# Optimization experiments

Hardware: AMD Instinct MI355X
Metric: run time of the kernel (lower is better)

The kernel has to match this reference:

```python
import jax, jax.numpy as jnp
from jax import lax
import numpy as np

PARAM_SPECS = [
    ("w1", (16, 15, 5, 5)), ("b1", (16,)),
    ("w2", (32, 16, 3, 3)), ("b2", (32,)),
    ("w3", (32, 32, 3, 3)), ("b3", (32,)),
    ("w4", (32, 32, 3, 3)), ("b4", (32,)),
    ("w5", (64, 32, 3, 3)), ("b5", (64,)),
    ("w6", (32, 96, 3, 3)), ("b6", (32,)),
    ("w7", (32, 64, 3, 3)), ("b7", (32,)),
    ("w8", (32, 64, 3, 3)), ("b8", (32,)),
    ("w9", (64, 48, 3, 3)), ("b9", (64,)),
    ("wi", (16, 15, 3, 3)), ("bi", (16,)),
    ("wo", (3, 16, 3, 3)), ("bo", (3,)),
]


def conv2d(x, w, b, pad):
    y = lax.conv_general_dilated(x, w, (1, 1), [(pad, pad), (pad, pad)],
                                 dimension_numbers=("NCHW", "OIHW", "NCHW"))
    return y + b[None, :, None, None]


def maxpool2(x):
    return lax.reduce_window(x, -jnp.inf, lax.max, (1, 1, 2, 2), (1, 1, 2, 2), "VALID")


def upsample(x, hw):
    # bilinear, half-pixel centers == torch align_corners=False
    B, C = x.shape[:2]
    return jax.image.resize(x, (B, C, hw[0], hw[1]), method="bilinear")


def dcnn(img, p):
    x1 = jax.nn.relu(conv2d(img, p["w1"], p["b1"], 2))
    x2 = jax.nn.relu(conv2d(maxpool2(x1), p["w2"], p["b2"], 1))
    x3 = jax.nn.relu(conv2d(maxpool2(x2), p["w3"], p["b3"], 1))
    x4 = jax.nn.relu(conv2d(maxpool2(x3), p["w4"], p["b4"], 1))
    x5 = jax.nn.relu(conv2d(maxpool2(x4), p["w5"], p["b5"], 1))
    x6 = jax.nn.relu(conv2d(jnp.concatenate([upsample(x5, x4.shape[-2:]), x4], 1), p["w6"], p["b6"], 1))
    x7 = jax.nn.relu(conv2d(jnp.concatenate([upsample(x6, x3.shape[-2:]), x3], 1), p["w7"], p["b7"], 1))
    x8 = jax.nn.relu(conv2d(jnp.concatenate([upsample(x7, x2.shape[-2:]), x2], 1), p["w8"], p["b8"], 1))
    x9 = conv2d(jnp.concatenate([upsample(x8, x1.shape[-2:]), x1], 1), p["w9"], p["b9"], 1)
    return x9


def lrnn_op(X, P, axis, flip):
    # h_k = (1-P_k)*X_k + P_k*h_{k-1}, scanned along `axis`.
    # For reverse directions the torch code stacks hidden states in scan
    # order (spatially flipped) -> flip inputs, scan forward, keep order.
    if flip:
        X = jnp.flip(X, axis)
        P = jnp.flip(P, axis)
    xs = jnp.moveaxis(X, axis, 0)  # [L, B, 16, n]
    ps = jnp.moveaxis(P, axis, 0)

    def step(h, xp):
        x, p = xp
        h = (1.0 - p) * x + p * h
        return h, h

    h0 = jnp.zeros_like(xs[0])
    _, ys = lax.scan(step, h0, (xs, ps))
    return jnp.moveaxis(ys, 0, axis)


def lrnn_layer(x_in, fm):
    dirs = [(0, 3, False), (0, 3, True), (16, 2, False), (16, 2, True),
            (32, 3, False), (32, 3, True), (48, 2, False), (48, 2, True)]
    outs = [lrnn_op(x_in, fm[:, c:c + 16], axis, flip) for (c, axis, flip) in dirs]
    return jnp.max(jnp.stack(outs, axis=1), axis=1)


def setup_inputs() -> dict:
    key = jax.random.key(0)
    ks = jax.random.split(key, len(PARAM_SPECS) + 1)
    inp = {"img": jax.random.normal(ks[0], (8, 15, 256, 256), jnp.float32)}
    for i, (name, shape) in enumerate(PARAM_SPECS):
        inp[name] = jax.random.normal(ks[i + 1], shape, jnp.float32) * 0.05
    return inp


def reference(img, w1, b1, w2, b2, w3, b3, w4, b4, w5, b5, w6, b6, w7, b7,
              w8, b8, w9, b9, wi, bi, wo, bo):
    p = dict(w1=w1, b1=b1, w2=w2, b2=b2, w3=w3, b3=b3, w4=w4, b4=b4, w5=w5,
             b5=b5, w6=w6, b6=b6, w7=w7, b7=b7, w8=w8, b8=b8, w9=w9, b9=b9)
    fm = jnp.tanh(dcnn(img, p))          # [B,64,H,W]
    x_in = conv2d(img, wi, bi, 1)         # [B,16,H,W]
    out = lrnn_layer(x_in, fm)            # [B,16,H,W]
    return jax.nn.sigmoid(conv2d(out, wo, bo, 1))  # [B,3,H,W]
```

## Files before the change

### kernel.cpp

```cpp
#include <hip/hip_runtime.h>
#include <math.h>

typedef __attribute__((ext_vector_type(8)))  short bf16x8;
typedef __attribute__((ext_vector_type(8)))  unsigned short u16x8;
typedef __attribute__((ext_vector_type(16))) float f32x16;

__device__ __forceinline__ unsigned short f2bf(float f) {
    unsigned u = __float_as_uint(f);
    unsigned r = (u + 0x7FFFu + ((u >> 16) & 1u)) >> 16;
    return (unsigned short)r;
}
__device__ __forceinline__ float bf2f(unsigned short h) {
    return __uint_as_float(((unsigned)h) << 16);
}
__device__ __forceinline__ unsigned pack2(unsigned short a, unsigned short b) {
    return (unsigned)a | ((unsigned)b << 16);
}
__device__ __forceinline__ float fast_tanh(float x) {
    float e = __expf(2.f * x);
    return 1.f - 2.f / (e + 1.f);
}

__device__ __forceinline__ void bilin_setup(int y, int x, int Hi, int Wi,
                                            int& i00, int& i01, int& i10, int& i11,
                                            float& wy, float& wx)
{
    float fy = 0.5f * y - 0.25f;
    float fx = 0.5f * x - 0.25f;
    float y0f = floorf(fy), x0f = floorf(fx);
    wy = fy - y0f; wx = fx - x0f;
    int yA = (int)y0f, xA = (int)x0f;
    int yB = yA + 1, xB = xA + 1;
    yA = yA < 0 ? 0 : (yA > Hi - 1 ? Hi - 1 : yA);
    yB = yB < 0 ? 0 : (yB > Hi - 1 ? Hi - 1 : yB);
    xA = xA < 0 ? 0 : (xA > Wi - 1 ? Wi - 1 : xA);
    xB = xB < 0 ? 0 : (xB > Wi - 1 ? Wi - 1 : xB);
    i00 = yA * Wi + xA; i01 = yA * Wi + xB;
    i10 = yB * Wi + xA; i11 = yB * Wi + xB;
}

__device__ __forceinline__ void up2_setup(int v, int Hi, int& i0, int& i1, float& w)
{
    int a = (v - 1) >> 1;
    i0 = a < 0 ? 0 : a;
    int b = a + 1;
    i1 = b > Hi - 1 ? Hi - 1 : b;
    w = (v & 1) ? 0.25f : 0.75f;
}

__device__ __forceinline__ u16x8 bilin8(const unsigned short* __restrict__ sb,
                                        int i00, int i01, int i10, int i11,
                                        float wy, float wx, int stride)
{
    u16x8 v00 = *(const u16x8*)(sb + (size_t)i00 * stride);
    u16x8 v01 = *(const u16x8*)(sb + (size_t)i01 * stride);
    u16x8 v10 = *(const u16x8*)(sb + (size_t)i10 * stride);
    u16x8 v11 = *(const u16x8*)(sb + (size_t)i11 * stride);
    float w00 = (1.f - wy) * (1.f - wx), w01 = (1.f - wy) * wx;
    float w10 = wy * (1.f - wx),         w11 = wy * wx;
    u16x8 r;
#pragma unroll
    for (int j = 0; j < 8; ++j)
        r[j] = f2bf(w00 * bf2f(v00[j]) + w01 * bf2f(v01[j]) +
                    w10 * bf2f(v10[j]) + w11 * bf2f(v11[j]));
    return r;
}

__device__ const float ALPH[3][2][3][3] = {
    { { {0.f,0.f,0.f},      {0.f,1.f,0.f},       {0.f,0.75f,0.25f} },
      { {0.f,1.f,0.f},      {0.f,0.75f,0.25f},   {0.f,0.25f,0.75f} } },
    { { {0.75f,0.25f,0.f},  {0.25f,0.75f,0.f},   {0.f,0.75f,0.25f} },
      { {0.25f,0.75f,0.f},  {0.f,0.75f,0.25f},   {0.f,0.25f,0.75f} } },
    { { {0.75f,0.25f,0.f},  {0.25f,0.75f,0.f},   {0.f,1.f,0.f} },
      { {0.25f,0.75f,0.f},  {0.f,1.f,0.f},       {0.f,0.f,0.f} } }
};

__global__ void imgT_bf16(const float* __restrict__ img, unsigned short* __restrict__ dst)
{
    int idx = blockIdx.x * 256 + threadIdx.x;
    if (idx >= 8 * 256 * 256) return;
    int x = idx & 255, y = (idx >> 8) & 255, b = idx >> 16;
    unsigned short v[16];
#pragma unroll
    for (int c = 0; c < 15; ++c)
        v[c] = f2bf(img[(size_t)(b * 15 + c) * 65536 + y * 256 + x]);
    v[15] = 0;
    uint4 lo = make_uint4(pack2(v[0], v[1]), pack2(v[2], v[3]), pack2(v[4], v[5]), pack2(v[6], v[7]));
    uint4 hi = make_uint4(pack2(v[8], v[9]), pack2(v[10], v[11]), pack2(v[12], v[13]), pack2(v[14], v[15]));
    *(uint4*)(dst + (size_t)idx * 16)     = lo;
    *(uint4*)(dst + (size_t)idx * 16 + 8) = hi;
}

__device__ __forceinline__ void pack33(const float* __restrict__ w,
                                       unsigned short* __restrict__ dst,
                                       int i, int Cin, int Cout)
{
    int KST = Cin >> 4, MT = Cout >> 5;
    int j = i & 7;
    int lane = (i >> 3) & 63;
    int t = i >> 9;
    int mt = t % MT; t /= MT;
    int kst = t % KST;
    int s = t / KST;
    int oc = mt * 32 + (lane & 31);
    int ci = kst * 16 + (lane >> 5) * 8 + j;
    dst[i] = f2bf(w[(oc * Cin + ci) * 9 + s]);
}

__global__ void wprep_mega(const float* __restrict__ w9, const float* __restrict__ w8,
                           const float* __restrict__ w1, const float* __restrict__ wi,
                           const float* __restrict__ wo, const float* __restrict__ w2,
                           const float* __restrict__ w3, const float* __restrict__ w4,
                           const float* __restrict__ w5, const float* __restrict__ w6,
                           const float* __restrict__ w7,
                           unsigned short* __restrict__ wpk9, unsigned short* __restrict__ wpk8,
                           unsigned short* __restrict__ wpk1, unsigned short* __restrict__ wpki,
                           unsigned short* __restrict__ wpko, unsigned short* __restrict__ wpk2,
                           unsigned short* __restrict__ wpk3, unsigned short* __restrict__ wpk4,
                           unsigned short* __restrict__ wpk5, unsigned short* __restrict__ wpk6,
                           unsigned short* __restrict__ wpk7, unsigned short* __restrict__ wpk9e)
{
    int idx = blockIdx.x * 256 + threadIdx.x;
    if (idx < 27648)       pack33(w9, wpk9, idx, 48, 64);
    else if (idx < 46080)  pack33(w8, wpk8, idx - 27648, 64, 32);
    else if (idx < 58880) {
        int i = idx - 46080;
        int j = i & 7;
        int lane = (i >> 3) & 63;
        int s = i >> 9;
        int oc = lane & 31;
        int ci = (lane >> 5) * 8 + j;
        float v = 0.f;
        if (oc < 16 && ci < 15) v = w1[((oc * 15 + ci) * 5 + s / 5) * 5 + s % 5];
        wpk1[i] = f2bf(v);
    } else if (idx < 63488) {
        int i = idx - 58880;
        int j = i & 7;
        int lane = (i >> 3) & 63;
        int s = i >> 9;
        int oc = lane & 31;
        int ci = (lane >> 5) * 8 + j;
        float v = 0.f;
        if (oc < 16 && ci < 15) v = wi[((oc * 15 + ci) * 3 + s / 3) * 3 + s % 3];
        wpki[i] = f2bf(v);
    } else if (idx < 68096) {
        int i = idx - 63488;
        int j = i & 7;
        int lane = (i >> 3) & 63;
        int s = i >> 9;
        int oc = lane & 31;
        int ci = (lane >> 5) * 8 + j;
        float v = 0.f;
        if (oc < 3) v = wo[((oc * 16 + ci) * 3 + s / 3) * 3 + s % 3];
        wpko[i] = f2bf(v);
    }
    else if (idx < 72704)  pack33(w2, wpk2, idx - 68096, 16, 32);
    else if (idx < 81920)  pack33(w3, wpk3, idx - 72704, 32, 32);
    else if (idx < 91136)  pack33(w4, wpk4, idx - 81920, 32, 32);
    else if (idx < 109568) pack33(w5, wpk5, idx - 91136, 32, 64);
    else if (idx < 137216) pack33(w6, wpk6, idx - 109568, 96, 32);
    else if (idx < 155648) pack33(w7, wpk7, idx - 137216, 64, 32);
    else if (idx < 266240) {
        int i = idx - 155648;
        int j = i & 7;
        int lane = (i >> 3) & 63;
        int t = i >> 9;
        int half = t & 1; t >>= 1;
        int kst  = t & 1; t >>= 1;
        int s    = t % 9; t /= 9;
        int py   = t & 1;
        int cls  = t >> 1;
        int dr = s / 3, dx = s % 3;
        int oc = half * 32 + (lane & 31);
        int ci = kst * 16 + (lane >> 5) * 8 + j;
        float v = 0.f;
#pragma unroll
        for (int dy = 0; dy < 3; ++dy)
            v += ALPH[cls][py][dy][dr] * w9[((oc * 48 + ci) * 3 + dy) * 3 + dx];
        wpk9e[i] = f2bf(v);
    }
}

template<int CIN, int COUT, int H, int W, int ROWS, int POOL>
__global__ __launch_bounds__(256)
void convN_mfma(const unsigned short* __restrict__ in,
                const unsigned short* __restrict__ wpk,
                const float* __restrict__ bias,
                unsigned short* __restrict__ out)
{
    constexpr int G = CIN / 8;
    constexpr int KST = CIN / 16;
    constexpr int MT = COUT / 32;
    constexpr int TR = ROWS + 2;
    constexpr int TWd = W + 2;
    constexpr int PS = TR * TWd * 8 + 8;
    __shared__ __align__(16) unsigned short smem[G * PS];

    const int tid  = threadIdx.x;
    const int lane = tid & 63;
    const int wv   = tid >> 6;
    const int q    = lane >> 5;
    const int y0   = blockIdx.x * ROWS;
    const int b    = blockIdx.y;

    for (int i = tid; i < G * TR * TWd; i += 256) {
        int g = i % G;
        int u = (i / G) % TWd;
        int t = i / (G * TWd);
        int yg = y0 + t - 1, xg = u - 1;
        u16x8 v = {0, 0, 0, 0, 0, 0, 0, 0};
        if (yg >= 0 && yg < H && xg >= 0 && xg < W) {
            if (POOL) {
                const unsigned short* q0 =
                    in + (((size_t)(b * 2 * H + 2 * yg) * 2 * W + 2 * xg) * CIN + g * 8);
                u16x8 a0 = *(const u16x8*)q0;
                u16x8 a1 = *(const u16x8*)(q0 + CIN);
                u16x8 a2 = *(const u16x8*)(q0 + (size_t)2 * W * CIN);
                u16x8 a3 = *(const u16x8*)(q0 + (size_t)2 * W * CIN + CIN);
#pragma unroll
                for (int j = 0; j < 8; ++j)
                    v[j] = f2bf(fmaxf(fmaxf(bf2f(a0[j]), bf2f(a1[j])),
                                      fmaxf(bf2f(a2[j]), bf2f(a3[j]))));
            } else {
                v = *(const u16x8*)(in + (((size_t)(b * H + yg) * W + xg) * CIN + g * 8));
            }
        }
        *(u16x8*)(&smem[g * PS + (t * TWd + u) * 8]) = v;
    }
    __syncthreads();

    const int p = wv * 32 + (lane & 31);
    const int r = p / W;
    const int x = p % W;

    f32x16 acc[MT];
#pragma unroll
    for (int mt = 0; mt < MT; ++mt)
#pragma unroll
        for (int i = 0; i < 16; ++i) acc[mt][i] = 0.f;

    const unsigned short* wbase = wpk + lane * 8;

#pragma unroll
    for (int s = 0; s < 9; ++s) {
        const int dy = s / 3, dx = s % 3;
#pragma unroll
        for (int kst = 0; kst < KST; ++kst) {
            const int g = kst * 2 + q;
            bf16x8 bfrag = *(const bf16x8*)(&smem[g * PS + ((r + dy) * TWd + (x + dx)) * 8]);
#pragma unroll
            for (int mt = 0; mt < MT; ++mt) {
                bf16x8 a = *(const bf16x8*)(wbase + ((s * KST + kst) * MT + mt) * 512);
                acc[mt] = __builtin_amdgcn_mfma_f32_32x32x16_bf16(a, bfrag, acc[mt], 0, 0, 0);
            }
        }
    }

    size_t base = ((size_t)(b * H + y0 + r) * W + x) * COUT;
#pragma unroll
    for (int mt = 0; mt < MT; ++mt)
#pragma unroll
        for (int rg = 0; rg < 4; ++rg) {
            int oc = mt * 32 + 8 * rg + 4 * q;
            unsigned short s0 = f2bf(fmaxf(acc[mt][rg * 4 + 0] + bias[oc + 0], 0.f));
            unsigned short s1 = f2bf(fmaxf(acc[mt][rg * 4 + 1] + bias[oc + 1], 0.f));
            unsigned short s2 = f2bf(fmaxf(acc[mt][rg * 4 + 2] + bias[oc + 2], 0.f));
            unsigned short s3 = f2bf(fmaxf(acc[mt][rg * 4 + 3] + bias[oc + 3], 0.f));
            *(uint2*)(out + base + oc) = make_uint2(pack2(s0, s1), pack2(s2, s3));
        }
}

template<int UPC, int CSKIP, int COUT, int H, int W, int ROWS>
__global__ __launch_bounds__(256)
void convU_mfma(const unsigned short* __restrict__ up,
                const unsigned short* __restrict__ skip,
                const unsigned short* __restrict__ wpk,
                const float* __restrict__ bias,
                unsigned short* __restrict__ out)
{
    constexpr int CIN = UPC + CSKIP;
    constexpr int G = CIN / 8;
    constexpr int GU = UPC / 8;
    constexpr int KST = CIN / 16;
    constexpr int MT = COUT / 32;
    constexpr int TR = ROWS + 2;
    constexpr int TWd = W + 2;
    constexpr int PS = TR * TWd * 8 + 8;
    __shared__ __align__(16) unsigned short smem[G * PS];

    const int tid  = threadIdx.x;
    const int lane = tid & 63;
    const int wv   = tid >> 6;
    const int q    = lane >> 5;
    const int y0   = blockIdx.x * ROWS;
    const int b    = blockIdx.y;

    for (int i = tid; i < G * TR * TWd; i += 256) {
        int g = i % G;
        int u = (i / G) % TWd;
        int t = i / (G * TWd);
        int yg = y0 + t - 1, xg = u - 1;
        u16x8 v = {0, 0, 0, 0, 0, 0, 0, 0};
        if (yg >= 0 && yg < H && xg >= 0 && xg < W) {
            if (g < GU) {
                int i00, i01, i10, i11; float wy, wx;
                bilin_setup(yg, xg, H / 2, W / 2, i00, i01, i10, i11, wy, wx);
                v = bilin8(up + (size_t)b * (H / 2) * (W / 2) * UPC + g * 8,
                           i00, i01, i10, i11, wy, wx, UPC);
            } else {
                v = *(const u16x8*)(skip + (((size_t)(b * H + yg) * W + xg) * CSKIP
                                            + (g - GU) * 8));
            }
        }
        *(u16x8*)(&smem[g * PS + (t * TWd + u) * 8]) = v;
    }
    __syncthreads();

    const int p = wv * 32 + (lane & 31);
    const int r = p / W;
    const int x = p % W;

    f32x16 acc[MT];
#pragma unroll
    for (int mt = 0; mt < MT; ++mt)
#pragma unroll
        for (int i = 0; i < 16; ++i) acc[mt][i] = 0.f;

    const unsigned short* wbase = wpk + lane * 8;

#pragma unroll
    for (int s = 0; s < 9; ++s) {
        const int dy = s / 3, dx = s % 3;
#pragma unroll
        for (int kst = 0; kst < KST; ++kst) {
            const int g = kst * 2 + q;
            bf16x8 bfrag = *(const bf16x8*)(&smem[g * PS + ((r + dy) * TWd + (x + dx)) * 8]);
#pragma unroll
            for (int mt = 0; mt < MT; ++mt) {
                bf16x8 a = *(const bf16x8*)(wbase + ((s * KST + kst) * MT + mt) * 512);
                acc[mt] = __builtin_amdgcn_mfma_f32_32x32x16_bf16(a, bfrag, acc[mt], 0, 0, 0);
            }
        }
    }

    size_t base = ((size_t)(b * H + y0 + r) * W + x) * COUT;
#pragma unroll
    for (int mt = 0; mt < MT; ++mt)
#pragma unroll
        for (int rg = 0; rg < 4; ++rg) {
            int oc = mt * 32 + 8 * rg + 4 * q;
            unsigned short s0 = f2bf(fmaxf(acc[mt][rg * 4 + 0] + bias[oc + 0], 0.f));
            unsigned short s1 = f2bf(fmaxf(acc[mt][rg * 4 + 1] + bias[oc + 1], 0.f));
            unsigned short s2 = f2bf(fmaxf(acc[mt][rg * 4 + 2] + bias[oc + 2], 0.f));
            unsigned short s3 = f2bf(fmaxf(acc[mt][rg * 4 + 3] + bias[oc + 3], 0.f));
            *(uint2*)(out + base + oc) = make_uint2(pack2(s0, s1), pack2(s2, s3));
        }
}

__global__ __launch_bounds__(256)
void conv1i_mfma(const unsigned short* __restrict__ imgT,
                 const unsigned short* __restrict__ wpk1,
                 const unsigned short* __restrict__ wpki,
                 const float* __restrict__ b1, const float* __restrict__ bi,
                 unsigned short* __restrict__ x1t, unsigned short* __restrict__ xin)
{
    __shared__ __align__(16) unsigned short smem[2 * 5 * 132 * 8];

    const int tid  = threadIdx.x;
    const int lane = tid & 63;
    const int wv   = tid >> 6;
    const int n    = lane & 31;
    const int q    = lane >> 5;
    const int y    = blockIdx.x >> 1;
    const int x0   = (blockIdx.x & 1) * 128;
    const int b    = blockIdx.y;

    for (int i = tid; i < 5 * 132 * 2; i += 256) {
        int r   = i / 264;
        int rem = i - r * 264;
        int xi  = rem >> 1;
        int g   = rem & 1;
        int yg = y + r - 2;
        int xg = x0 - 2 + xi;
        uint4 v = make_uint4(0, 0, 0, 0);
        if (yg >= 0 && yg < 256 && xg >= 0 && xg < 256)
            v = *(const uint4*)(imgT + (((size_t)(b * 256 + yg) * 256 + xg) * 16 + g * 8));
        *(uint4*)(&smem[((g * 5 + r) * 132 + xi) * 8]) = v;
    }
    __syncthreads();

    f32x16 acc1, acci;
#pragma unroll
    for (int i = 0; i < 16; ++i) { acc1[i] = 0.f; acci[i] = 0.f; }

    const int pxl = wv * 32 + n;
    const unsigned short* wb1 = wpk1 + lane * 8;
    const unsigned short* wbi = wpki + lane * 8;

#pragma unroll
    for (int s = 0; s < 25; ++s) {
        const int dy = s / 5, dx = s % 5;
        bf16x8 bfrag = *(const bf16x8*)(&smem[((q * 5 + dy) * 132 + pxl + dx) * 8]);
        bf16x8 a = *(const bf16x8*)(wb1 + s * 512);
        acc1 = __builtin_amdgcn_mfma_f32_32x32x16_bf16(a, bfrag, acc1, 0, 0, 0);
    }
#pragma unroll
    for (int s = 0; s < 9; ++s) {
        const int dy = s / 3, dx = s % 3;
        bf16x8 bfrag = *(const bf16x8*)(&smem[((q * 5 + dy + 1) * 132 + pxl + dx + 1) * 8]);
        bf16x8 a = *(const bf16x8*)(wbi + s * 512);
        acci = __builtin_amdgcn_mfma_f32_32x32x16_bf16(a, bfrag, acci, 0, 0, 0);
    }

    const int px = x0 + pxl;
    size_t base1 = ((size_t)(b * 256 + y) * 256 + px) * 16;
#pragma unroll
    for (int rg = 0; rg < 2; ++rg) {
        int oc = 8 * rg + 4 * q;
        unsigned short s0 = f2bf(fmaxf(acc1[rg * 4 + 0] + b1[oc + 0], 0.f));
        unsigned short s1 = f2bf(fmaxf(acc1[rg * 4 + 1] + b1[oc + 1], 0.f));
        unsigned short s2 = f2bf(fmaxf(acc1[rg * 4 + 2] + b1[oc + 2], 0.f));
        unsigned short s3 = f2bf(fmaxf(acc1[rg * 4 + 3] + b1[oc + 3], 0.f));
        *(uint2*)(x1t + base1 + oc) = make_uint2(pack2(s0, s1), pack2(s2, s3));
    }
#pragma unroll
    for (int reg = 0; reg < 8; ++reg) {
        int row = (reg & 3) + 8 * (reg >> 2) + 4 * q;
        xin[((size_t)(b * 16 + row) * 256 + y) * 256 + px] = f2bf(acci[reg] + bi[row]);
    }
}

__global__ __launch_bounds__(256)
void conv8_mfma(const unsigned short* __restrict__ x7t,
                const unsigned short* __restrict__ x2t,
                const unsigned short* __restrict__ wpk8,
                const float* __restrict__ bias,
                unsigned short* __restrict__ x8t)
{
    constexpr int PS8 = 4 * 66 * 8 + 8;
    __shared__ __align__(16) unsigned short smem[8 * PS8];

    const int tid  = threadIdx.x;
    const int lane = tid & 63;
    const int wv   = tid >> 6;
    const int n    = lane & 31;
    const int q    = lane >> 5;
    const int x0   = (blockIdx.x & 1) * 64;
    const int yp   = blockIdx.x >> 1;
    const int b    = blockIdx.y;

    for (int i = tid; i < 8 * 4 * 66; i += 256) {
        int t   = i / 528;
        int rem = i - t * 528;
        int xi  = rem >> 3;
        int g   = rem & 7;
        int yg = 2 * yp + t - 1;
        int xg = x0 - 1 + xi;
        u16x8 v = {0, 0, 0, 0, 0, 0, 0, 0};
        if (yg >= 0 && yg < 128 && xg >= 0 && xg < 128) {
            if (g < 4) {
                int iy0, iy1, ix0, ix1; float wy, wx;
                up2_setup(yg, 64, iy0, iy1, wy);
                up2_setup(xg, 64, ix0, ix1, wx);
                v = bilin8(x7t + (size_t)b * 64 * 64 * 32 + g * 8,
                           iy0 * 64 + ix0, iy0 * 64 + ix1,
                           iy1 * 64 + ix0, iy1 * 64 + ix1, wy, wx, 32);
            } else {
                v = *(const u16x8*)(x2t + (((size_t)(b * 128 + yg) * 128 + xg) * 32
                                           + (g - 4) * 8));
            }
        }
        *(u16x8*)(&smem[g * PS8 + (t * 66 + xi) * 8]) = v;
    }
    __syncthreads();

    const int rr  = wv >> 1;
    const int pxl = (wv & 1) * 32 + n;

    f32x16 acc;
#pragma unroll
    for (int i = 0; i < 16; ++i) acc[i] = 0.f;

    const unsigned short* wbase = wpk8 + lane * 8;

#pragma unroll
    for (int s = 0; s < 9; ++s) {
        const int dy = s / 3, dx = s % 3;
#pragma unroll
        for (int kst = 0; kst < 4; ++kst) {
            const int g = kst * 2 + q;
            bf16x8 bfrag = *(const bf16x8*)(&smem[g * PS8 + ((rr + dy) * 66 + pxl + dx) * 8]);
            bf16x8 a = *(const bf16x8*)(wbase + (s * 4 + kst) * 512);
            acc = __builtin_amdgcn_mfma_f32_32x32x16_bf16(a, bfrag, acc, 0, 0, 0);
        }
    }

    size_t base = ((size_t)(b * 128 + 2 * yp + rr) * 128 + x0 + pxl) * 32;
#pragma unroll
    for (int rg = 0; rg < 4; ++rg) {
        int oc0 = 8 * rg + 4 * q;
        unsigned short s0 = f2bf(fmaxf(acc[rg * 4 + 0] + bias[oc0 + 0], 0.f));
        unsigned short s1 = f2bf(fmaxf(acc[rg * 4 + 1] + bias[oc0 + 1], 0.f));
        unsigned short s2 = f2bf(fmaxf(acc[rg * 4 + 2] + bias[oc0 + 2], 0.f));
        unsigned short s3 = f2bf(fmaxf(acc[rg * 4 + 3] + bias[oc0 + 3], 0.f));
        *(uint2*)(x8t + base + oc0) = make_uint2(pack2(s0, s1), pack2(s2, s3));
    }
}

__global__ __launch_bounds__(256)
void conv9f_mfma(const unsigned short* __restrict__ x8t,
                 const unsigned short* __restrict__ x1t,
                 const unsigned short* __restrict__ wpk,
                 const unsigned short* __restrict__ wpk9e,
                 const float* __restrict__ bias,
                 unsigned short* __restrict__ fm)
{
    constexpr int PS8X = 3 * 66 * 8 + 8;
    constexpr int PS1  = 4 * 66 * 8 + 8;
    constexpr int X1OFF = 4 * PS8X;
    __shared__ __align__(16) unsigned short smem[4 * PS8X + 2 * PS1];

    const int tid  = threadIdx.x;
    const int lane = tid & 63;
    const int wv   = tid >> 6;
    const int n    = lane & 31;
    const int q    = lane >> 5;
    const int x0   = (blockIdx.x & 3) * 64;
    const int yp   = blockIdx.x >> 2;
    const int b    = blockIdx.y;

    for (int i = tid; i < 792 + 528; i += 256) {
        if (i < 792) {
            int g   = i & 3;
            int rem = i >> 2;
            int xi  = rem % 66;
            int t8  = rem / 66;
            int r   = yp - 1 + t8;
            int xg  = x0 - 1 + xi;
            u16x8 v = {0, 0, 0, 0, 0, 0, 0, 0};
            if (r >= 0 && r < 128 && xg >= 0 && xg < 256) {
                int ix0, ix1; float wx;
                up2_setup(xg, 128, ix0, ix1, wx);
                const unsigned short* S = x8t + ((size_t)(b * 128 + r) * 128) * 32 + g * 8;
                u16x8 a0 = *(const u16x8*)(S + ix0 * 32);
                u16x8 a1 = *(const u16x8*)(S + ix1 * 32);
                float w1x = 1.f - wx;
#pragma unroll
                for (int j = 0; j < 8; ++j)
                    v[j] = f2bf(w1x * bf2f(a0[j]) + wx * bf2f(a1[j]));
            }
            *(u16x8*)(&smem[g * PS8X + (t8 * 66 + xi) * 8]) = v;
        } else {
            int jI  = i - 792;
            int g   = jI & 1;
            int rem = jI >> 1;
            int xi  = rem % 66;
            int t   = rem / 66;
            int yg  = 2 * yp + t - 1;
            int xg  = x0 - 1 + xi;
            uint4 v = make_uint4(0, 0, 0, 0);
            if (yg >= 0 && yg < 256 && xg >= 0 && xg < 256)
                v = *(const uint4*)(x1t + (((size_t)(b * 256 + yg) * 256 + xg) * 16 + g * 8));
            *(uint4*)(&smem[X1OFF + g * PS1 + (t * 66 + xi) * 8]) = v;
        }
    }
    __syncthreads();

    const int rr  = wv >> 1;
    const int pxl = (wv & 1) * 32 + n;

    f32x16 acc0, acc1;
#pragma unroll
    for (int i = 0; i < 16; ++i) { acc0[i] = 0.f; acc1[i] = 0.f; }

    const int cls = (yp == 0) ? 0 : ((yp == 127) ? 2 : 1);
    const unsigned short* wE  = wpk9e + (size_t)(cls * 2 + rr) * 18432 + lane * 8;
    const unsigned short* w2b = wpk + lane * 8;

#pragma unroll
    for (int s = 0; s < 9; ++s) {
        const int dr = s / 3, dxx = s % 3;
#pragma unroll
        for (int kst = 0; kst < 2; ++kst) {
            const int g = kst * 2 + q;
            bf16x8 bfrag = *(const bf16x8*)(&smem[g * PS8X + (dr * 66 + pxl + dxx) * 8]);
            bf16x8 a0 = *(const bf16x8*)(wE + ((s * 2 + kst) * 2 + 0) * 512);
            bf16x8 a1 = *(const bf16x8*)(wE + ((s * 2 + kst) * 2 + 1) * 512);
            acc0 = __builtin_amdgcn_mfma_f32_32x32x16_bf16(a0, bfrag, acc0, 0, 0, 0);
            acc1 = __builtin_amdgcn_mfma_f32_32x32x16_bf16(a1, bfrag, acc1, 0, 0, 0);
        }
        {
            bf16x8 bfrag = *(const bf16x8*)(&smem[X1OFF + q * PS1 + ((rr + dr) * 66 + pxl + dxx) * 8]);
            bf16x8 a0 = *(const bf16x8*)(w2b + ((s * 3 + 2) * 2 + 0) * 512);
            bf16x8 a1 = *(const bf16x8*)(w2b + ((s * 3 + 2) * 2 + 1) * 512);
            acc0 = __builtin_amdgcn_mfma_f32_32x32x16_bf16(a0, bfrag, acc0, 0, 0, 0);
            acc1 = __builtin_amdgcn_mfma_f32_32x32x16_bf16(a1, bfrag, acc1, 0, 0, 0);
        }
    }

    __syncthreads();
    unsigned short* lout = smem;
    const int pb = rr * 64 + pxl + q * 512;
#pragma unroll
    for (int reg = 0; reg < 16; ++reg) {
        const int rbase = (reg & 3) + 8 * (reg >> 2);
        lout[rbase * 128 + pb]        = f2bf(fast_tanh(acc0[reg] + bias[rbase + 4 * q]));
        lout[(rbase + 32) * 128 + pb] = f2bf(fast_tanh(acc1[reg] + bias[rbase + 4 * q + 32]));
    }
    __syncthreads();

    const size_t fmb = (size_t)b * 64 * 65536 + (size_t)(2 * yp) * 256 + x0;
    for (int i = tid; i < 1024; i += 256) {
        int oc  = i >> 4;
        int p0  = (i & 15) * 8;
        int rr2 = p0 >> 6;
        int pl  = p0 & 63;
        uint4 v = *(const uint4*)(lout + oc * 128 + p0);
        *(uint4*)(fm + fmb + (size_t)oc * 65536 + rr2 * 256 + pl) = v;
    }
}

__device__ __forceinline__ int X2C(int x) { return x + (x >> 5); }

__global__ __launch_bounds__(256)
void lrnn_w_seg(const unsigned short* __restrict__ X, const unsigned short* __restrict__ FM,
                unsigned short* __restrict__ rnnW)
{
    __shared__ float tx[3][16][264];
    __shared__ unsigned short outm[2][16][256];
    __shared__ float segres[2][16][8][4];
    __shared__ float hin[2][16][8][2];

    const int tid = threadIdx.x;
    const int bid = blockIdx.x;
    const int yt = bid & 15;
    const int c  = (bid >> 4) & 15;
    const int b  = bid >> 8;
    const int y0 = yt * 16;

    const size_t xb  = ((size_t)(b * 16 + c) * 256 + y0) * 256;
    const size_t p1b = ((size_t)(b * 64 + c) * 256 + y0) * 256;
    const size_t p2b = ((size_t)(b * 64 + 32 + c) * 256 + y0) * 256;

    for (int i = tid; i < 1536; i += 256) {
        int s = i >> 9;
        int r = i & 511;
        int y = r >> 5;
        int g = r & 31;
        const unsigned short* sp = (s == 0) ? (X + xb) : (s == 1 ? FM + p1b : FM + p2b);
        u16x8 v = *(const u16x8*)(sp + (size_t)y * 256 + g * 8);
        int c0 = X2C(g * 8);
#pragma unroll
        for (int j = 0; j < 8; ++j) tx[s][y][c0 + j] = bf2f(v[j]);
    }
    __syncthreads();

    const int y  = tid & 15;
    const int sg = (tid >> 4) & 7;
    const int d  = tid >> 7;

    {
        float h1 = 0.f, h2 = 0.f, A1 = 1.f, A2 = 1.f;
        if (d == 0) {
            int cs = X2C(sg * 32);
#pragma unroll
            for (int i = 0; i < 32; ++i) {
                float xv = tx[0][y][cs + i], p1 = tx[1][y][cs + i], p2 = tx[2][y][cs + i];
                h1 = fmaf(p1, h1 - xv, xv); A1 *= p1;
                h2 = fmaf(p2, h2 - xv, xv); A2 *= p2;
            }
        } else {
            int cs = X2C(255 - sg * 32);
#pragma unroll
            for (int i = 0; i < 32; ++i) {
                float xv = tx[0][y][cs - i], p1 = tx[1][y][cs - i], p2 = tx[2][y][cs - i];
                h1 = fmaf(p1, h1 - xv, xv); A1 *= p1;
                h2 = fmaf(p2, h2 - xv, xv); A2 *= p2;
            }
        }
        segres[d][y][sg][0] = h1; segres[d][y][sg][1] = A1;
        segres[d][y][sg][2] = h2; segres[d][y][sg][3] = A2;
    }
    __syncthreads();

    if (tid < 32) {
        int yy = tid & 15, dd = tid >> 4;
        float c1 = 0.f, c2 = 0.f;
        for (int s = 0; s < 8; ++s) {
            hin[dd][yy][s][0] = c1;
            hin[dd][yy][s][1] = c2;
            c1 = segres[dd][yy][s][0] + segres[dd][yy][s][1] * c1;
            c2 = segres[dd][yy][s][2] + segres[dd][yy][s][3] * c2;
        }
    }
    __syncthreads();

    {
        float h1 = hin[d][y][sg][0], h2 = hin[d][y][sg][1];
        if (d == 0) {
            int cs = X2C(sg * 32);
            int xs = sg * 32;
#pragma unroll
            for (int i = 0; i < 32; ++i) {
                float xv = tx[0][y][cs + i], p1 = tx[1][y][cs + i], p2 = tx[2][y][cs + i];
                h1 = fmaf(p1, h1 - xv, xv);
                h2 = fmaf(p2, h2 - xv, xv);
                outm[0][y][xs + i] = f2bf(fmaxf(h1, h2));
            }
        } else {
            int cs = X2C(255 - sg * 32);
#pragma unroll
            for (int i = 0; i < 32; ++i) {
                int t = sg * 32 + i;
                float xv = tx[0][y][cs - i], p1 = tx[1][y][cs - i], p2 = tx[2][y][cs - i];
                h1 = fmaf(p1, h1 - xv, xv);
                h2 = fmaf(p2, h2 - xv, xv);
                outm[1][y][t] = f2bf(fmaxf(h1, h2));
            }
        }
    }
    __syncthreads();

    for (int i = tid; i < 4096; i += 256) {
        int x = i & 255, yy = i >> 8;
        float m = fmaxf(bf2f(outm[0][yy][x]), bf2f(outm[1][yy][x]));
        rnnW[xb + (size_t)yy * 256 + x] = f2bf(m);
    }
}

__global__ __launch_bounds__(256)
void lrnn_h_seg(const unsigned short* __restrict__ X, const unsigned short* __restrict__ FM,
                unsigned short* __restrict__ rnnH)
{
    __shared__ float tx[3][264][17];
    __shared__ unsigned short outm[2][256][16];
    __shared__ float segres[2][16][8][4];
    __shared__ float hin[2][16][8][2];

    const int tid = threadIdx.x;
    const int bid = blockIdx.x;
    const int xt = bid & 15;
    const int c  = (bid >> 4) & 15;
    const int b  = bid >> 8;
    const int x0 = xt * 16;

    const size_t xb  = (size_t)(b * 16 + c) * 65536 + x0;
    const size_t p1b = (size_t)(b * 64 + 16 + c) * 65536 + x0;
    const size_t p2b = (size_t)(b * 64 + 48 + c) * 65536 + x0;

    for (int i = tid; i < 1536; i += 256) {
        int s = i >> 9;
        int r = i & 511;
        int y = r >> 1;
        int g = r & 1;
        const unsigned short* sp = (s == 0) ? (X + xb) : (s == 1 ? FM + p1b : FM + p2b);
        u16x8 v = *(const u16x8*)(sp + (size_t)y * 256 + g * 8);
        int pr = y + (y >> 5);
#pragma unroll
        for (int j = 0; j < 8; ++j) tx[s][pr][g * 8 + j] = bf2f(v[j]);
    }
    __syncthreads();

    const int x  = tid & 15;
    const int sg = (tid >> 4) & 7;
    const int d  = tid >> 7;

    {
        float h1 = 0.f, h2 = 0.f, A1 = 1.f, A2 = 1.f;
        if (d == 0) {
            int rs = X2C(sg * 32);
#pragma unroll
            for (int i = 0; i < 32; ++i) {
                float xv = tx[0][rs + i][x], p1 = tx[1][rs + i][x], p2 = tx[2][rs + i][x];
                h1 = fmaf(p1, h1 - xv, xv); A1 *= p1;
                h2 = fmaf(p2, h2 - xv, xv); A2 *= p2;
            }
        } else {
            int rs = X2C(255 - sg * 32);
#pragma unroll
            for (int i = 0; i < 32; ++i) {
                float xv = tx[0][rs - i][x], p1 = tx[1][rs - i][x], p2 = tx[2][rs - i][x];
                h1 = fmaf(p1, h1 - xv, xv); A1 *= p1;
                h2 = fmaf(p2, h2 - xv, xv); A2 *= p2;
            }
        }
        segres[d][x][sg][0] = h1; segres[d][x][sg][1] = A1;
        segres[d][x][sg][2] = h2; segres[d][x][sg][3] = A2;
    }
    __syncthreads();

    if (tid < 32) {
        int xx = tid & 15, dd = tid >> 4;
        float c1 = 0.f, c2 = 0.f;
        for (int s = 0; s < 8; ++s) {
            hin[dd][xx][s][0] = c1;
            hin[dd][xx][s][1] = c2;
            c1 = segres[dd][xx][s][0] + segres[dd][xx][s][1] * c1;
            c2 = segres[dd][xx][s][2] + segres[dd][xx][s][3] * c2;
        }
    }
    __syncthreads();

    {
        float h1 = hin[d][x][sg][0], h2 = hin[d][x][sg][1];
        if (d == 0) {
            int rs = X2C(sg * 32);
            int ys = sg * 32;
#pragma unroll
            for (int i = 0; i < 32; ++i) {
                float xv = tx[0][rs + i][x], p1 = tx[1][rs + i][x], p2 = tx[2][rs + i][x];
                h1 = fmaf(p1, h1 - xv, xv);
                h2 = fmaf(p2, h2 - xv, xv);
                outm[0][ys + i][x] = f2bf(fmaxf(h1, h2));
            }
        } else {
            int rs = X2C(255 - sg * 32);
#pragma unroll
            for (int i = 0; i < 32; ++i) {
                int t = sg * 32 + i;
                float xv = tx[0][rs - i][x], p1 = tx[1][rs - i][x], p2 = tx[2][rs - i][x];
                h1 = fmaf(p1, h1 - xv, xv);
                h2 = fmaf(p2, h2 - xv, xv);
                outm[1][t][x] = f2bf(fmaxf(h1, h2));
            }
        }
    }
    __syncthreads();

    for (int i = tid; i < 4096; i += 256) {
        int xx = i & 15, yy = i >> 4;
        float m = fmaxf(bf2f(outm[0][yy][xx]), bf2f(outm[1][yy][xx]));
        rnnH[xb + (size_t)yy * 256 + xx] = f2bf(m);
    }
}

__global__ __launch_bounds__(256)
void convo_mfma(const unsigned short* __restrict__ rnnW,
                const unsigned short* __restrict__ rnnH,
                const unsigned short* __restrict__ wpko,
                const float* __restrict__ bo,
                float* __restrict__ outp)
{
    __shared__ __align__(16) unsigned short smem[2 * 3 * 130 * 8];

    const int tid  = threadIdx.x;
    const int lane = tid & 63;
    const int wv   = tid >> 6;
    const int n    = lane & 31;
    const int q    = lane >> 5;
    const int y    = blockIdx.x >> 1;
    const int x0   = (blockIdx.x & 1) * 128;
    const int b    = blockIdx.y;

    for (int i = tid; i < 3 * 16 * 130; i += 256) {
        int xi = i % 130;
        int t  = i / 130;
        int ch = t & 15;
        int r  = t >> 4;
        int yg = y + r - 1;
        int xg = x0 - 1 + xi;
        unsigned short m = 0;
        if (yg >= 0 && yg < 256 && xg >= 0 && xg < 256) {
            size_t off = (size_t)(b * 16 + ch) * 65536 + yg * 256 + xg;
            m = f2bf(fmaxf(bf2f(rnnW[off]), bf2f(rnnH[off])));
        }
        int g = ch >> 3, j = ch & 7;
        smem[((g * 3 + r) * 130 + xi) * 8 + j] = m;
    }
    __syncthreads();

    f32x16 acc;
#pragma unroll
    for (int i = 0; i < 16; ++i) acc[i] = 0.f;

    const int pxl = wv * 32 + n;
    const unsigned short* wbase = wpko + lane * 8;

#pragma unroll
    for (int s = 0; s < 9; ++s) {
        const int dy = s / 3, dx = s % 3;
        bf16x8 bfrag = *(const bf16x8*)(&smem[((q * 3 + dy) * 130 + pxl + dx) * 8]);
        bf16x8 a = *(const bf16x8*)(wbase + s * 512);
        acc = __builtin_amdgcn_mfma_f32_32x32x16_bf16(a, bfrag, acc, 0, 0, 0);
    }

    const int px = x0 + pxl;
    if (q == 0) {
#pragma unroll
        for (int oc = 0; oc < 3; ++oc) {
            float r = acc[oc] + bo[oc];
            outp[((size_t)(b * 3 + oc) * 256 + y) * 256 + px] = 1.f / (1.f + __expf(-r));
        }
    }
}

extern "C" void kernel_launch(void* const* d_in, const int* in_sizes, int n_in,
                              void* d_out, int out_size, void* d_ws, size_t ws_size,
                              hipStream_t stream)
{
    const float* img = (const float*)d_in[0];
    const float* w1 = (const float*)d_in[1];  const float* b1 = (const float*)d_in[2];
    const float* w2 = (const float*)d_in[3];  const float* b2 = (const float*)d_in[4];
    const float* w3 = (const float*)d_in[5];  const float* b3 = (const float*)d_in[6];
    const float* w4 = (const float*)d_in[7];  const float* b4 = (const float*)d_in[8];
    const float* w5 = (const float*)d_in[9];  const float* b5 = (const float*)d_in[10];
    const float* w6 = (const float*)d_in[11]; const float* b6 = (const float*)d_in[12];
    const float* w7 = (const float*)d_in[13]; const float* b7 = (const float*)d_in[14];
    const float* w8 = (const float*)d_in[15]; const float* b8 = (const float*)d_in[16];
    const float* w9 = (const float*)d_in[17]; const float* b9 = (const float*)d_in[18];
    const float* wi = (const float*)d_in[19]; const float* bi = (const float*)d_in[20];
    const float* wo = (const float*)d_in[21]; const float* bo = (const float*)d_in[22];

    char* wsb = (char*)d_ws;
    const size_t MB = (size_t)(1u << 20);
    unsigned short* imgT  = (unsigned short*)(wsb);
    unsigned short* x1t   = (unsigned short*)(wsb + 16 * MB);
    unsigned short* x2t   = (unsigned short*)(wsb + 32 * MB);
    unsigned short* x3t   = (unsigned short*)(wsb + 40 * MB);
    unsigned short* x4t   = (unsigned short*)(wsb + 42 * MB);
    unsigned short* x5t   = (unsigned short*)(wsb + 43 * MB);
    unsigned short* x6t   = (unsigned short*)(wsb + 46 * MB);
    unsigned short* x7t   = (unsigned short*)(wsb + 51 * MB);
    unsigned short* x8t   = (unsigned short*)(wsb + 70 * MB);
    unsigned short* fm16  = (unsigned short*)(wsb + 112 * MB);
    unsigned short* xin16 = (unsigned short*)(wsb + 176 * MB);
    unsigned short* rnnW  = (unsigned short*)(wsb);
    unsigned short* rnnH  = (unsigned short*)(wsb + 16 * MB);
    unsigned short* wpk9 = (unsigned short*)(wsb + 192 * MB);
    unsigned short* wpk8 = wpk9 + 27648;
    unsigned short* wpk1 = wpk8 + 18432;
    unsigned short* wpki = wpk1 + 12800;
    unsigned short* wpko = wpki + 4608;
    unsigned short* wpk2 = wpko + 4608;
    unsigned short* wpk3 = wpk2 + 4608;
    unsigned short* wpk4 = wpk3 + 9216;
    unsigned short* wpk5 = wpk4 + 9216;
    unsigned short* wpk6 = wpk5 + 18432;
    unsigned short* wpk7 = wpk6 + 27648;
    unsigned short* wpk9e = wpk7 + 18432;
    float* outp = (float*)d_out;

    wprep_mega<<<1040, 256, 0, stream>>>(w9, w8, w1, wi, wo, w2, w3, w4, w5, w6, w7,
                                         wpk9, wpk8, wpk1, wpki, wpko,
                                         wpk2, wpk3, wpk4, wpk5, wpk6, wpk7, wpk9e);
    imgT_bf16<<<2048, 256, 0, stream>>>(img, imgT);

    { dim3 grd(512, 8);
      conv1i_mfma<<<grd, 256, 0, stream>>>(imgT, wpk1, wpki, b1, bi, x1t, xin16); }

    convN_mfma<16, 32, 128, 128, 1, 1><<<dim3(128, 8), 256, 0, stream>>>(x1t, wpk2, b2, x2t);
    convN_mfma<32, 32, 64, 64, 2, 1><<<dim3(32, 8), 256, 0, stream>>>(x2t, wpk3, b3, x3t);
    convN_mfma<32, 32, 32, 32, 4, 1><<<dim3(8, 8), 256, 0, stream>>>(x3t, wpk4, b4, x4t);
    convN_mfma<32, 64, 16, 16, 8, 1><<<dim3(2, 8), 256, 0, stream>>>(x4t, wpk5, b5, x5t);

    convU_mfma<64, 32, 32, 32, 32, 4><<<dim3(8, 8), 256, 0, stream>>>(x5t, x4t, wpk6, b6, x6t);
    convU_mfma<32, 32, 32, 64, 64, 2><<<dim3(32, 8), 256, 0, stream>>>(x6t, x3t, wpk7, b7, x7t);
    { dim3 grd(128, 8);
      conv8_mfma<<<grd, 256, 0, stream>>>(x7t, x2t, wpk8, b8, x8t); }

    { dim3 grd(512, 8);
      conv9f_mfma<<<grd, 256, 0, stream>>>(x8t, x1t, wpk9, wpk9e, b9, fm16); }

    lrnn_w_seg<<<2048, 256, 0, stream>>>(xin16, fm16, rnnW);
    lrnn_h_seg<<<2048, 256, 0, stream>>>(xin16, fm16, rnnH);

    { dim3 grd(512, 8);
      convo_mfma<<<grd, 256, 0, stream>>>(rnnW, rnnH, wpko, bo, outp); }
}
```

Measured before the change: 387.0 us.

## Fold vertical upsample into conv8 weights and vectorize convo max staging

conv8 now stages only horizontally-interpolated low-res x7 rows and uses precomputed weights that fold the vertical bilinear interpolation into the 3x3 filter (per boundary class and row parity), as already done for conv9. This removes the 4-tap bilinear gather from the staging loop. Separately, the convo staging loop reads rnnW/rnnH eight pixels at a time with vector loads instead of per-element scalar loads. The folded weights add a larger weight-prep workload and round the combined weights to bf16, which can shift numerics slightly.

```diff
diff --git a/kernel.cpp b/kernel.cpp
--- a/kernel.cpp
+++ b/kernel.cpp
@@ -118,7 +118,8 @@
                            unsigned short* __restrict__ wpko, unsigned short* __restrict__ wpk2,
                            unsigned short* __restrict__ wpk3, unsigned short* __restrict__ wpk4,
                            unsigned short* __restrict__ wpk5, unsigned short* __restrict__ wpk6,
-                           unsigned short* __restrict__ wpk7, unsigned short* __restrict__ wpk9e)
+                           unsigned short* __restrict__ wpk7, unsigned short* __restrict__ wpk9e,
+                           unsigned short* __restrict__ wpk8e)
 {
     int idx = blockIdx.x * 256 + threadIdx.x;
     if (idx < 27648)       pack33(w9, wpk9, idx, 48, 64);
@@ -179,6 +180,24 @@
             v += ALPH[cls][py][dy][dr] * w9[((oc * 48 + ci) * 3 + dy) * 3 + dx];
         wpk9e[i] = f2bf(v);
     }
+    else if (idx < 321536) {
+        int i = idx - 266240;
+        int j = i & 7;
+        int lane = (i >> 3) & 63;
+        int t = i >> 9;
+        int kst = t & 1; t >>= 1;
+        int s   = t % 9; t /= 9;
+        int py  = t & 1;
+        int cls = t >> 1;
+        int dr = s / 3, dx = s % 3;
+        int oc = lane & 31;
+        int ci = kst * 16 + (lane >> 5) * 8 + j;
+        float v = 0.f;
+#pragma unroll
+        for (int dy = 0; dy < 3; ++dy)
+            v += ALPH[cls][py][dy][dr] * w8[((oc * 64 + ci) * 3 + dy) * 3 + dx];
+        wpk8e[i] = f2bf(v);
+    }
 }
 
 template<int CIN, int COUT, int H, int W, int ROWS, int POOL>
@@ -434,11 +453,14 @@
 void conv8_mfma(const unsigned short* __restrict__ x7t,
                 const unsigned short* __restrict__ x2t,
                 const unsigned short* __restrict__ wpk8,
+                const unsigned short* __restrict__ wpk8e,
                 const float* __restrict__ bias,
                 unsigned short* __restrict__ x8t)
 {
-    constexpr int PS8 = 4 * 66 * 8 + 8;
-    __shared__ __align__(16) unsigned short smem[8 * PS8];
+    constexpr int PSU = 3 * 66 * 8 + 8;
+    constexpr int PSS = 4 * 66 * 8 + 8;
+    constexpr int SOFF = 4 * PSU;
+    __shared__ __align__(16) unsigned short smem[4 * PSU + 4 * PSS];
 
     const int tid  = threadIdx.x;
     const int lane = tid & 63;
@@ -449,28 +471,40 @@
     const int yp   = blockIdx.x >> 1;
     const int b    = blockIdx.y;
 
-    for (int i = tid; i < 8 * 4 * 66; i += 256) {
-        int t   = i / 528;
-        int rem = i - t * 528;
-        int xi  = rem >> 3;
-        int g   = rem & 7;
-        int yg = 2 * yp + t - 1;
-        int xg = x0 - 1 + xi;
-        u16x8 v = {0, 0, 0, 0, 0, 0, 0, 0};
-        if (yg >= 0 && yg < 128 && xg >= 0 && xg < 128) {
-            if (g < 4) {
-                int iy0, iy1, ix0, ix1; float wy, wx;
-                up2_setup(yg, 64, iy0, iy1, wy);
+    for (int i = tid; i < 792 + 1056; i += 256) {
+        if (i < 792) {
+            int g   = i & 3;
+            int rem = i >> 2;
+            int xi  = rem % 66;
+            int t8  = rem / 66;
+            int r   = yp - 1 + t8;
+            int xg  = x0 - 1 + xi;
+            u16x8 v = {0, 0, 0, 0, 0, 0, 0, 0};
+            if (r >= 0 && r < 64 && xg >= 0 && xg < 128) {
+                int ix0, ix1; float wx;
                 up2_setup(xg, 64, ix0, ix1, wx);
-                v = bilin8(x7t + (size_t)b * 64 * 64 * 32 + g * 8,
-                           iy0 * 64 + ix0, iy0 * 64 + ix1,
-                           iy1 * 64 + ix0, iy1 * 64 + ix1, wy, wx, 32);
-            } else {
-                v = *(const u16x8*)(x2t + (((size_t)(b * 128 + yg) * 128 + xg) * 32
-                                           + (g - 4) * 8));
-            }
-        }
-        *(u16x8*)(&smem[g * PS8 + (t * 66 + xi) * 8]) = v;
+                const unsigned short* S = x7t + ((size_t)(b * 64 + r) * 64) * 32 + g * 8;
+                u16x8 a0 = *(const u16x8*)(S + ix0 * 32);
+                u16x8 a1 = *(const u16x8*)(S + ix1 * 32);
+                float w1x = 1.f - wx;
+#pragma unroll
+                for (int j = 0; j < 8; ++j)
+                    v[j] = f2bf(w1x * bf2f(a0[j]) + wx * bf2f(a1[j]));
+            }
+            *(u16x8*)(&smem[g * PSU + (t8 * 66 + xi) * 8]) = v;
+        } else {
+            int jI  = i - 792;
+            int g   = jI & 3;
+            int rem = jI >> 2;
+            int xi  = rem % 66;
+            int t   = rem / 66;
+            int yg  = 2 * yp + t - 1;
+            int xg  = x0 - 1 + xi;
+            uint4 v = make_uint4(0, 0, 0, 0);
+            if (yg >= 0 && yg < 128 && xg >= 0 && xg < 128)
+                v = *(const uint4*)(x2t + (((size_t)(b * 128 + yg) * 128 + xg) * 32 + g * 8));
+            *(uint4*)(&smem[SOFF + g * PSS + (t * 66 + xi) * 8]) = v;
+        }
     }
     __syncthreads();
 
@@ -481,16 +515,25 @@
 #pragma unroll
     for (int i = 0; i < 16; ++i) acc[i] = 0.f;
 
-    const unsigned short* wbase = wpk8 + lane * 8;
+    const int cls = (yp == 0) ? 0 : ((yp == 63) ? 2 : 1);
+    const unsigned short* wE = wpk8e + (size_t)(cls * 2 + rr) * 9216 + lane * 8;
+    const unsigned short* wS = wpk8 + lane * 8;
 
 #pragma unroll
     for (int s = 0; s < 9; ++s) {
-        const int dy = s / 3, dx = s % 3;
-#pragma unroll
-        for (int kst = 0; kst < 4; ++kst) {
+        const int dr = s / 3, dxx = s % 3;
+#pragma unroll
+        for (int kst = 0; kst < 2; ++kst) {
             const int g = kst * 2 + q;
-            bf16x8 bfrag = *(const bf16x8*)(&smem[g * PS8 + ((rr + dy) * 66 + pxl + dx) * 8]);
-            bf16x8 a = *(const bf16x8*)(wbase + (s * 4 + kst) * 512);
+            bf16x8 bfrag = *(const bf16x8*)(&smem[g * PSU + (dr * 66 + pxl + dxx) * 8]);
+            bf16x8 a = *(const bf16x8*)(wE + (s * 2 + kst) * 512);
+            acc = __builtin_amdgcn_mfma_f32_32x32x16_bf16(a, bfrag, acc, 0, 0, 0);
+        }
+#pragma unroll
+        for (int kst = 0; kst < 2; ++kst) {
+            const int g = kst * 2 + q;
+            bf16x8 bfrag = *(const bf16x8*)(&smem[SOFF + g * PSS + ((rr + dr) * 66 + pxl + dxx) * 8]);
+            bf16x8 a = *(const bf16x8*)(wS + (s * 4 + kst + 2) * 512);
             acc = __builtin_amdgcn_mfma_f32_32x32x16_bf16(a, bfrag, acc, 0, 0, 0);
         }
     }
@@ -852,20 +895,46 @@
     const int x0   = (blockIdx.x & 1) * 128;
     const int b    = blockIdx.y;
 
-    for (int i = tid; i < 3 * 16 * 130; i += 256) {
-        int xi = i % 130;
-        int t  = i / 130;
-        int ch = t & 15;
-        int r  = t >> 4;
-        int yg = y + r - 1;
-        int xg = x0 - 1 + xi;
-        unsigned short m = 0;
-        if (yg >= 0 && yg < 256 && xg >= 0 && xg < 256) {
-            size_t off = (size_t)(b * 16 + ch) * 65536 + yg * 256 + xg;
-            m = f2bf(fmaxf(bf2f(rnnW[off]), bf2f(rnnH[off])));
-        }
+    for (int i = tid; i < 3 * 16 * 17; i += 256) {
+        int ch  = i & 15;
+        int t   = i >> 4;
+        int c   = t % 17;
+        int r   = t / 17;
+        int xi0 = c * 8;
+        int yg  = y + r - 1;
         int g = ch >> 3, j = ch & 7;
-        smem[((g * 3 + r) * 130 + xi) * 8 + j] = m;
+        unsigned short* sb = &smem[((g * 3 + r) * 130) * 8 + j];
+        if (yg >= 0 && yg < 256) {
+            size_t off = (size_t)(b * 16 + ch) * 65536 + (size_t)yg * 256;
+            int xg0 = x0 - 1 + xi0;
+            if (xg0 >= 0 && xg0 + 7 < 256 && xi0 + 7 < 130) {
+                u16x8 a  = *(const u16x8*)(rnnW + off + xg0);
+                u16x8 bv = *(const u16x8*)(rnnH + off + xg0);
+#pragma unroll
+                for (int k = 0; k < 8; ++k)
+                    sb[(xi0 + k) * 8] = bf2f(a[k]) >= bf2f(bv[k]) ? a[k] : bv[k];
+            } else {
+#pragma unroll
+                for (int k = 0; k < 8; ++k) {
+                    int xi = xi0 + k;
+                    if (xi >= 130) break;
+                    int xg = x0 - 1 + xi;
+                    unsigned short m = 0;
+                    if (xg >= 0 && xg < 256) {
+                        unsigned short a = rnnW[off + xg], bvv = rnnH[off + xg];
+                        m = bf2f(a) >= bf2f(bvv) ? a : bvv;
+                    }
+                    sb[xi * 8] = m;
+                }
+            }
+        } else {
+#pragma unroll
+            for (int k = 0; k < 8; ++k) {
+                int xi = xi0 + k;
+                if (xi >= 130) break;
+                sb[xi * 8] = 0;
+            }
+        }
     }
     __syncthreads();
 
@@ -938,11 +1007,13 @@
     unsigned short* wpk6 = wpk5 + 18432;
     unsigned short* wpk7 = wpk6 + 27648;
     unsigned short* wpk9e = wpk7 + 18432;
+    unsigned short* wpk8e = wpk9e + 110592;
     float* outp = (float*)d_out;
 
-    wprep_mega<<<1040, 256, 0, stream>>>(w9, w8, w1, wi, wo, w2, w3, w4, w5, w6, w7,
+    wprep_mega<<<1256, 256, 0, stream>>>(w9, w8, w1, wi, wo, w2, w3, w4, w5, w6, w7,
                                          wpk9, wpk8, wpk1, wpki, wpko,
-                                         wpk2, wpk3, wpk4, wpk5, wpk6, wpk7, wpk9e);
+                                         wpk2, wpk3, wpk4, wpk5, wpk6, wpk7,
+                                         wpk9e, wpk8e);
     imgT_bf16<<<2048, 256, 0, stream>>>(img, imgT);
 
     { dim3 grd(512, 8);
@@ -956,7 +1027,7 @@
     convU_mfma<64, 32, 32, 32, 32, 4><<<dim3(8, 8), 256, 0, stream>>>(x5t, x4t, wpk6, b6, x6t);
     convU_mfma<32, 32, 32, 64, 64, 2><<<dim3(32, 8), 256, 0, stream>>>(x6t, x3t, wpk7, b7, x7t);
     { dim3 grd(128, 8);
-      conv8_mfma<<<grd, 256, 0, stream>>>(x7t, x2t, wpk8, b8, x8t); }
+      conv8_mfma<<<grd, 256, 0, stream>>>(x7t, x2t, wpk8, wpk8e, b8, x8t); }
 
     { dim3 grd(512, 8);
       conv9f_mfma<<<grd, 256, 0, stream>>>(x8t, x1t, wpk9, wpk9e, b9, fm16); }
```

New measurement: 413.8 us. +6.9%, slower.
